# Performance work log

Hardware: AMD Instinct MI355X
Metric: run time of the kernel (lower is better)

The kernel has to match this reference:

```python
import jax, jax.numpy as jnp
import numpy as np

HEADS = 8
HEAD_DIM = 80
TEXT_LEN = 77


def setup_inputs() -> dict:
    key = jax.random.key(0)
    ks = jax.random.split(key, 10)
    B, S, QD, CD, ID = 16, 4096, 640, 768, 640
    NV = 10
    s = 0.02
    return {
        "x": jax.random.normal(ks[0], (B, S, QD), jnp.float32),
        "enc": jax.random.normal(ks[1], (B, TEXT_LEN + NV, CD), jnp.float32),
        "Wq": jax.random.normal(ks[2], (QD, ID), jnp.float32) * s,
        "Wvq": jax.random.normal(ks[3], (QD, ID), jnp.float32) * s,
        "Wk": jax.random.normal(ks[4], (CD, ID), jnp.float32) * s,
        "Wv": jax.random.normal(ks[5], (CD, ID), jnp.float32) * s,
        "Wvk": jax.random.normal(ks[6], (CD, ID), jnp.float32) * s,
        "Wvv": jax.random.normal(ks[7], (CD, ID), jnp.float32) * s,
        "Wo": jax.random.normal(ks[8], (ID, QD), jnp.float32) * s,
        "bo": jnp.zeros((QD,), jnp.float32),
    }


def reference(x, enc, Wq, Wvq, Wk, Wv, Wvk, Wvv, Wo, bo):
    # x: [B, S, query_dim]; enc: [B, 77 + Nv, cross_dim]
    B, S, _ = x.shape
    H, D = HEADS, HEAD_DIM
    scale = 1.0 / jnp.sqrt(jnp.asarray(D, x.dtype))

    text_feats = enc[:, :TEXT_LEN]      # [B, 77, CD]
    visual_feats = enc[:, TEXT_LEN:]    # [B, Nv, CD]

    tq = (x @ Wq).reshape(B, S, H, D)
    vq = (x @ Wvq).reshape(B, S, H, D)
    tk = (text_feats @ Wk).reshape(B, TEXT_LEN, H, D)
    tv = (text_feats @ Wv).reshape(B, TEXT_LEN, H, D)
    vk = (visual_feats @ Wvk).reshape(B, -1, H, D)
    vv = (visual_feats @ Wvv).reshape(B, -1, H, D)

    # separate score blocks, then concat along key dim
    text_scores = scale * jnp.einsum("bqhd,bkhd->bhqk", tq, tk)
    visual_scores = scale * jnp.einsum("bqhd,bkhd->bhqk", vq, vk)
    scores = jnp.concatenate([text_scores, visual_scores], axis=-1)  # [B,H,S,Kt+Kv]
    probs = jax.nn.softmax(scores, axis=-1)

    value = jnp.concatenate([tv, vv], axis=1)  # [B, Kt+Kv, H, D]
    out = jnp.einsum("bhqk,bkhd->bqhd", probs, value).reshape(B, S, H * D)
    return out @ Wo + bo
```

## Files before the change

kernel.cpp:

```cpp
#include <hip/hip_runtime.h>

typedef __attribute__((ext_vector_type(8))) short short8;
typedef __attribute__((ext_vector_type(4))) float f32x4;
typedef __attribute__((ext_vector_type(4))) int int4v;

typedef const __attribute__((address_space(1))) void* gas_t;
typedef __attribute__((address_space(3))) void* las_t;

__device__ __forceinline__ unsigned short f2bf(float f) {
  unsigned int u = __float_as_uint(f);
  u += 0x7fffu + ((u >> 16) & 1u);
  return (unsigned short)(u >> 16);
}

__global__ void cvt_bf16_kernel(const float* __restrict__ in,
                                unsigned short* __restrict__ out, int n) {
  int i = (blockIdx.x * 256 + threadIdx.x) * 4;
  if (i + 3 < n) {
    float4 v = *(const float4*)(in + i);
    ushort4 r;
    r.x = f2bf(v.x); r.y = f2bf(v.y); r.z = f2bf(v.z); r.w = f2bf(v.w);
    *(ushort4*)(out + i) = r;
  }
}

__global__ void transpose_cvt_kernel(const float* __restrict__ W,
                                     unsigned short* __restrict__ Wt,
                                     int K, int N) {
  __shared__ float t[32][33];
  int tx = threadIdx.x & 31, ty = threadIdx.x >> 5;
  int k0 = blockIdx.x * 32, n0 = blockIdx.y * 32;
  #pragma unroll
  for (int i = 0; i < 32; i += 8)
    t[ty + i][tx] = W[(size_t)(k0 + ty + i) * N + n0 + tx];
  __syncthreads();
  #pragma unroll
  for (int i = 0; i < 32; i += 8)
    Wt[(size_t)(n0 + ty + i) * K + k0 + tx] = f2bf(t[tx][ty + i]);
}

__global__ void vtrans_kernel(const unsigned short* __restrict__ KV,
                              unsigned short* __restrict__ VtG) {
  int idx = blockIdx.x * 256 + threadIdx.x;
  if (idx >= 16 * 8 * 80 * 96) return;
  int k = idx % 96;
  int d = (idx / 96) % 80;
  int h = (idx / (96 * 80)) % 8;
  int b = idx / (96 * 80 * 8);
  unsigned short v = 0;
  if (k < 87) {
    int base = (k < 77) ? 640 : 1920;
    v = KV[(size_t)(b * 87 + k) * 2560 + base + h * 80 + d];
  }
  VtG[idx] = v;
}

template<bool F32OUT>
__global__ __launch_bounds__(256, 2) void gemm_bt_kernel(
    const unsigned short* __restrict__ A,
    const unsigned short* __restrict__ Bt,
    void* __restrict__ Cptr, const float* __restrict__ bias,
    int M, int N, int K, int NT) {
  __shared__ __align__(16) unsigned short smem[2 * 128 * 64];
  unsigned short* As = smem;
  unsigned short* Bs = smem + 128 * 64;

  const int tid  = threadIdx.x;
  const int wave = tid >> 6, lane = tid & 63;
  const int lrow = lane & 15, quad = lane >> 4;

  const int nwg = gridDim.x;
  const int qch = nwg >> 3, rch = nwg & 7;
  const int xcd = blockIdx.x & 7;
  const int wgid = (xcd < rch ? xcd * (qch + 1)
                              : rch * (qch + 1) + (xcd - rch) * qch)
                 + (blockIdx.x >> 3);
  const int row0 = (wgid / NT) * 128, col0 = (wgid % NT) * 128;

  const int wm = (wave >> 1) * 64, wn = (wave & 1) * 64;
  const int srow = lane >> 3;
  const int scol = (lane & 7) * 8;

  f32x4 zero = {0.f, 0.f, 0.f, 0.f};
  f32x4 acc[4][4];
  #pragma unroll
  for (int mi = 0; mi < 4; ++mi)
    #pragma unroll
    for (int ni = 0; ni < 4; ++ni) acc[mi][ni] = zero;

  for (int k0 = 0; k0 < K; k0 += 64) {
    #pragma unroll
    for (int i = 0; i < 4; ++i) {
      int r = (wave * 4 + i) * 8 + srow;
      int ga = row0 + r; if (ga > M - 1) ga = M - 1;
      const unsigned short* gA = A + (size_t)ga * K + k0 + scol;
      __builtin_amdgcn_global_load_lds((gas_t)gA, (las_t)(As + r * 64 + scol), 16, 0, 0);
      const unsigned short* gB = Bt + (size_t)(col0 + r) * K + k0 + scol;
      __builtin_amdgcn_global_load_lds((gas_t)gB, (las_t)(Bs + r * 64 + scol), 16, 0, 0);
    }
    __syncthreads();
    #pragma unroll
    for (int kk = 0; kk < 64; kk += 32) {
      short8 av[4], bv[4];
      #pragma unroll
      for (int mi = 0; mi < 4; ++mi)
        av[mi] = *(const short8*)(As + (wm + mi * 16 + lrow) * 64 + kk + quad * 8);
      #pragma unroll
      for (int ni = 0; ni < 4; ++ni)
        bv[ni] = *(const short8*)(Bs + (wn + ni * 16 + lrow) * 64 + kk + quad * 8);
      #pragma unroll
      for (int mi = 0; mi < 4; ++mi)
        #pragma unroll
        for (int ni = 0; ni < 4; ++ni)
          acc[mi][ni] = __builtin_amdgcn_mfma_f32_16x16x32_bf16(av[mi], bv[ni], acc[mi][ni], 0, 0, 0);
    }
    __syncthreads();
  }

  if (F32OUT) {
    float* C = (float*)Cptr;
    #pragma unroll
    for (int mi = 0; mi < 4; ++mi)
      #pragma unroll
      for (int ni = 0; ni < 4; ++ni) {
        int col = col0 + wn + ni * 16 + lrow;
        float bv = bias[col];
        #pragma unroll
        for (int r = 0; r < 4; ++r) {
          int row = row0 + wm + mi * 16 + quad * 4 + r;
          if (row < M) C[(size_t)row * N + col] = acc[mi][ni][r] + bv;
        }
      }
  } else {
    unsigned short* C = (unsigned short*)Cptr;
    unsigned short* Cw = smem + wave * 4096;
    #pragma unroll
    for (int mi = 0; mi < 4; ++mi)
      #pragma unroll
      for (int ni = 0; ni < 4; ++ni)
        #pragma unroll
        for (int r = 0; r < 4; ++r)
          Cw[(mi * 16 + quad * 4 + r) * 64 + ni * 16 + lrow] = f2bf(acc[mi][ni][r]);
    #pragma unroll
    for (int it = 0; it < 8; ++it) {
      int row = it * 8 + (lane >> 3);
      int c8  = (lane & 7) * 8;
      int grow = row0 + wm + row;
      if (grow < M) {
        int4v v = *(const int4v*)(Cw + row * 64 + c8);
        *(int4v*)(C + (size_t)grow * N + col0 + wn + c8) = v;
      }
    }
  }
}

__global__ __launch_bounds__(256, 3) void attn_kernel(
    const unsigned short* __restrict__ Q,
    const unsigned short* __restrict__ KV,
    const unsigned short* __restrict__ VtG,
    unsigned short* __restrict__ O) {
  constexpr int KS = 168;
  constexpr int PS = 104;
  __shared__ __align__(16) unsigned short smem[96 * KS + 80 * PS];
  unsigned short* Ke = smem;
  unsigned short* Vt = smem + 96 * KS;
  unsigned short* P  = smem;

  const int tid = threadIdx.x;
  const int wave = tid >> 6, lane = tid & 63;
  const int lrow = lane & 15, quad = lane >> 4;
  const int qt = blockIdx.x, h = blockIdx.y, b = blockIdx.z;
  const size_t qbase = (size_t)(b * 4096 + qt * 64);

  const unsigned short* vg = VtG + (size_t)(b * 8 + h) * 80 * 96;
  for (int idx = tid; idx < 80 * 12; idx += 256) {
    int r = idx / 12, c = idx % 12;
    *(int4v*)(Vt + r * PS + c * 8) = *(const int4v*)(vg + r * 96 + c * 8);
  }
  for (int idx = tid; idx < 96 * 20; idx += 256) {
    int r = idx / 20, c = idx % 20;
    int4v v = {0, 0, 0, 0};
    if (r < 87) {
      if (r < 77 && c < 10)
        v = *(const int4v*)(KV + (size_t)(b * 87 + r) * 2560 + h * 80 + c * 8);
      else if (r >= 77 && c >= 10)
        v = *(const int4v*)(KV + (size_t)(b * 87 + r) * 2560 + 1280 + h * 80 + (c - 10) * 8);
    }
    *(int4v*)(Ke + r * KS + c * 8) = v;
  }

  const unsigned short* Qrow = Q + (qbase + wave * 16 + lrow) * 1280;
  short8 qfrag[5];
  #pragma unroll
  for (int kc = 0; kc < 5; ++kc) {
    int j = kc * 32 + quad * 8;
    int gcol = h * 80 + j + (j >= 80 ? 560 : 0);
    qfrag[kc] = *(const short8*)(Qrow + gcol);
  }
  __syncthreads();

  f32x4 zero = {0.f, 0.f, 0.f, 0.f};
  f32x4 s[6];
  #pragma unroll
  for (int nt = 0; nt < 6; ++nt) s[nt] = zero;
  #pragma unroll
  for (int kc = 0; kc < 5; ++kc) {
    #pragma unroll
    for (int nt = 0; nt < 6; ++nt) {
      short8 bb = *(const short8*)(Ke + (nt * 16 + lrow) * KS + kc * 32 + quad * 8);
      s[nt] = __builtin_amdgcn_mfma_f32_16x16x32_bf16(qfrag[kc], bb, s[nt], 0, 0, 0);
    }
  }

  const float scale = 0.11180339887498949f;
  float mrow[4] = {-1e30f, -1e30f, -1e30f, -1e30f};
  #pragma unroll
  for (int nt = 0; nt < 6; ++nt) {
    bool valid = (nt * 16 + lrow) < 87;
    #pragma unroll
    for (int r = 0; r < 4; ++r) {
      float v = valid ? s[nt][r] * scale : -1e30f;
      s[nt][r] = v;
      mrow[r] = fmaxf(mrow[r], v);
    }
  }
  #pragma unroll
  for (int off = 1; off < 16; off <<= 1)
    #pragma unroll
    for (int r = 0; r < 4; ++r)
      mrow[r] = fmaxf(mrow[r], __shfl_xor(mrow[r], off, 64));
  float lsum[4] = {0.f, 0.f, 0.f, 0.f};
  #pragma unroll
  for (int nt = 0; nt < 6; ++nt)
    #pragma unroll
    for (int r = 0; r < 4; ++r) {
      float p = __expf(s[nt][r] - mrow[r]);
      s[nt][r] = p;
      lsum[r] += p;
    }
  #pragma unroll
  for (int off = 1; off < 16; off <<= 1)
    #pragma unroll
    for (int r = 0; r < 4; ++r)
      lsum[r] += __shfl_xor(lsum[r], off, 64);
  float inv[4];
  #pragma unroll
  for (int r = 0; r < 4; ++r) inv[r] = 1.0f / lsum[r];

  __syncthreads();

  #pragma unroll
  for (int nt = 0; nt < 6; ++nt)
    #pragma unroll
    for (int r = 0; r < 4; ++r)
      P[(wave * 16 + quad * 4 + r) * PS + nt * 16 + lrow] = f2bf(s[nt][r] * inv[r]);

  f32x4 o[5];
  #pragma unroll
  for (int nt = 0; nt < 5; ++nt) o[nt] = zero;
  #pragma unroll
  for (int kc = 0; kc < 3; ++kc) {
    short8 a = *(const short8*)(P + (wave * 16 + lrow) * PS + kc * 32 + quad * 8);
    #pragma unroll
    for (int nt = 0; nt < 5; ++nt) {
      short8 bb = *(const short8*)(Vt + (nt * 16 + lrow) * PS + kc * 32 + quad * 8);
      o[nt] = __builtin_amdgcn_mfma_f32_16x16x32_bf16(a, bb, o[nt], 0, 0, 0);
    }
  }

  unsigned short* Ow = P + wave * 16 * PS;
  #pragma unroll
  for (int nt = 0; nt < 5; ++nt)
    #pragma unroll
    for (int r = 0; r < 4; ++r)
      Ow[(quad * 4 + r) * PS + nt * 16 + lrow] = f2bf(o[nt][r]);
  for (int idx = lane; idx < 160; idx += 64) {
    int r = idx / 10, c = idx % 10;
    *(int4v*)(O + (qbase + wave * 16 + r) * 640 + h * 80 + c * 8) =
        *(const int4v*)(Ow + r * PS + c * 8);
  }
}

extern "C" void kernel_launch(void* const* d_in, const int* in_sizes, int n_in,
                              void* d_out, int out_size, void* d_ws, size_t ws_size,
                              hipStream_t stream) {
  const float* x   = (const float*)d_in[0];
  const float* enc = (const float*)d_in[1];
  const float* Wq  = (const float*)d_in[2];
  const float* Wvq = (const float*)d_in[3];
  const float* Wk  = (const float*)d_in[4];
  const float* Wv  = (const float*)d_in[5];
  const float* Wvk = (const float*)d_in[6];
  const float* Wvv = (const float*)d_in[7];
  const float* Wo  = (const float*)d_in[8];
  const float* bo  = (const float*)d_in[9];
  float* out = (float*)d_out;
  char* ws = (char*)d_ws;

  unsigned short* Qall  = (unsigned short*)(ws);
  unsigned short* xbf   = (unsigned short*)(ws + 167772160ull);
  unsigned short* encbf = (unsigned short*)(ws + 251658240ull);
  unsigned short* KVall = (unsigned short*)(ws + 253796352ull);
  unsigned short* WqcT  = (unsigned short*)(ws + 260923392ull);
  unsigned short* WkvT  = (unsigned short*)(ws + 262561792ull);
  unsigned short* WoT   = (unsigned short*)(ws + 266493952ull);
  unsigned short* VtG   = WkvT;

  cvt_bf16_kernel<<<40960, 256, 0, stream>>>(x, xbf, 41943040);
  cvt_bf16_kernel<<<1044, 256, 0, stream>>>(enc, encbf, 1069056);

  transpose_cvt_kernel<<<dim3(20, 20), 256, 0, stream>>>(Wq,  WqcT,             640, 640);
  transpose_cvt_kernel<<<dim3(20, 20), 256, 0, stream>>>(Wvq, WqcT + 640 * 640, 640, 640);
  transpose_cvt_kernel<<<dim3(24, 20), 256, 0, stream>>>(Wk,  WkvT,              768, 640);
  transpose_cvt_kernel<<<dim3(24, 20), 256, 0, stream>>>(Wv,  WkvT + 640 * 768,  768, 640);
  transpose_cvt_kernel<<<dim3(24, 20), 256, 0, stream>>>(Wvk, WkvT + 1280 * 768, 768, 640);
  transpose_cvt_kernel<<<dim3(24, 20), 256, 0, stream>>>(Wvv, WkvT + 1920 * 768, 768, 640);
  transpose_cvt_kernel<<<dim3(20, 20), 256, 0, stream>>>(Wo,  WoT,              640, 640);

  gemm_bt_kernel<false><<<220, 256, 0, stream>>>(encbf, WkvT, KVall, nullptr, 1392, 2560, 768, 20);
  vtrans_kernel<<<3840, 256, 0, stream>>>(KVall, VtG);
  gemm_bt_kernel<false><<<5120, 256, 0, stream>>>(xbf, WqcT, Qall, nullptr, 65536, 1280, 640, 10);
  attn_kernel<<<dim3(64, 8, 16), 256, 0, stream>>>(Qall, KVall, VtG, xbf);
  gemm_bt_kernel<true><<<2560, 256, 0, stream>>>(xbf, WoT, out, bo, 65536, 640, 640, 5);
}
```

Measured before the change: 690.3 us.

## Add 256x256-tile 8-wave GEMM with 4-stage LDS pipeline for Q and output projections

Adds a new GEMM kernel that uses 256x256 output tiles, 512 threads, a 4-slot global_load_lds prefetch ring with three stages in flight, XCD-aware tile remapping and s_setprio around the MFMA blocks. The Q/visual-Q projection and the output projection now use this kernel instead of the 128-tile kernel. The aim is more operand reuse per byte loaded and better overlap of loads with compute on the large 65536-row GEMMs. In exchange it uses 128 KB of LDS and many accumulator registers per wave, which lowers occupancy. The output GEMM with N=640 leaves a partly empty last column tile, so some work is wasted.

```diff
diff --git a/kernel.cpp b/kernel.cpp
--- a/kernel.cpp
+++ b/kernel.cpp
@@ -143,6 +143,161 @@
           Cw[(mi * 16 + quad * 4 + r) * 64 + ni * 16 + lrow] = f2bf(acc[mi][ni][r]);
     #pragma unroll
     for (int it = 0; it < 8; ++it) {
+      int row = it * 8 + (lane >> 3);
+      int c8  = (lane & 7) * 8;
+      int grow = row0 + wm + row;
+      if (grow < M) {
+        int4v v = *(const int4v*)(Cw + row * 64 + c8);
+        *(int4v*)(C + (size_t)grow * N + col0 + wn + c8) = v;
+      }
+    }
+  }
+}
+
+template<bool F32OUT>
+__global__ __launch_bounds__(512, 2) void gemm256_kernel(
+    const unsigned short* __restrict__ A,
+    const unsigned short* __restrict__ Bt,
+    void* __restrict__ Cptr, const float* __restrict__ bias,
+    int M, int N, int K, int NT) {
+  __shared__ __align__(16) unsigned short smem[4 * 16384];
+
+  const int tid  = threadIdx.x;
+  const int wave = tid >> 6, lane = tid & 63;
+  const int lrow = lane & 15, quad = lane >> 4;
+
+  const int nwg = gridDim.x;
+  const int qch = nwg >> 3, rch = nwg & 7;
+  const int xcd = blockIdx.x & 7;
+  const int wgid = (xcd < rch ? xcd * (qch + 1)
+                              : rch * (qch + 1) + (xcd - rch) * qch)
+                 + (blockIdx.x >> 3);
+  const int row0 = (wgid / NT) * 256, col0 = (wgid % NT) * 256;
+
+  const int wm = (wave >> 2) * 128;
+  const int wn = (wave & 3) * 64;
+  const int NKT = K >> 5;
+
+  const unsigned short* gA[2];
+  const unsigned short* gB[2];
+  #pragma unroll
+  for (int j = 0; j < 2; ++j) {
+    int P = tid * 16 + j * 8192;
+    int lin = P ^ (((P >> 9) & 1) << 5);
+    int r = ((P >> 10) << 4) + ((lin >> 6) & 15);
+    int c = (lin & 63) >> 1;
+    int ga = row0 + r; if (ga > M - 1) ga = M - 1;
+    int gb = col0 + r; if (gb > N - 1) gb = N - 1;
+    gA[j] = A  + (size_t)ga * K + c;
+    gB[j] = Bt + (size_t)gb * K + c;
+  }
+
+  const int xorb = ((lrow >> 3) & 1) << 4;
+  int offA[8], offB[4];
+  #pragma unroll
+  for (int mi = 0; mi < 8; ++mi)
+    offA[mi] = (((((wm >> 4) + mi) << 9) + (lrow << 5) + (quad << 3))) ^ xorb;
+  #pragma unroll
+  for (int ni = 0; ni < 4; ++ni)
+    offB[ni] = (((((wn >> 4) + ni) << 9) + (lrow << 5) + (quad << 3))) ^ xorb;
+
+  f32x4 zero = {0.f, 0.f, 0.f, 0.f};
+  f32x4 acc[8][4];
+  #pragma unroll
+  for (int mi = 0; mi < 8; ++mi)
+    #pragma unroll
+    for (int ni = 0; ni < 4; ++ni) acc[mi][ni] = zero;
+
+  #pragma unroll
+  for (int t = 0; t < 3; ++t) {
+    unsigned short* slot = smem + (t & 3) * 16384;
+    #pragma unroll
+    for (int j = 0; j < 2; ++j)
+      __builtin_amdgcn_global_load_lds((gas_t)(gA[j] + t * 32),
+          (las_t)(slot + j * 4096 + tid * 8), 16, 0, 0);
+    #pragma unroll
+    for (int j = 0; j < 2; ++j)
+      __builtin_amdgcn_global_load_lds((gas_t)(gB[j] + t * 32),
+          (las_t)(slot + 8192 + j * 4096 + tid * 8), 16, 0, 0);
+  }
+
+  for (int t = 0; t < NKT; ++t) {
+    if (t + 2 < NKT)      asm volatile("s_waitcnt vmcnt(8)" ::: "memory");
+    else if (t + 1 < NKT) asm volatile("s_waitcnt vmcnt(4)" ::: "memory");
+    else                  asm volatile("s_waitcnt vmcnt(0)" ::: "memory");
+    asm volatile("s_barrier" ::: "memory");
+
+    const unsigned short* As = smem + (t & 3) * 16384;
+    const unsigned short* Bs = As + 8192;
+    const bool pf = (t + 3 < NKT);
+    unsigned short* nslot = smem + ((t + 3) & 3) * 16384;
+
+    short8 av0[4], bv[4];
+    #pragma unroll
+    for (int mi = 0; mi < 4; ++mi) av0[mi] = *(const short8*)(As + offA[mi]);
+    #pragma unroll
+    for (int ni = 0; ni < 4; ++ni) bv[ni] = *(const short8*)(Bs + offB[ni]);
+    if (pf) {
+      #pragma unroll
+      for (int j = 0; j < 2; ++j)
+        __builtin_amdgcn_global_load_lds((gas_t)(gA[j] + (t + 3) * 32),
+            (las_t)(nslot + j * 4096 + tid * 8), 16, 0, 0);
+    }
+    __builtin_amdgcn_s_setprio(1);
+    #pragma unroll
+    for (int mi = 0; mi < 4; ++mi)
+      #pragma unroll
+      for (int ni = 0; ni < 4; ++ni)
+        acc[mi][ni] = __builtin_amdgcn_mfma_f32_16x16x32_bf16(av0[mi], bv[ni], acc[mi][ni], 0, 0, 0);
+    __builtin_amdgcn_s_setprio(0);
+
+    short8 av1[4];
+    #pragma unroll
+    for (int mi = 0; mi < 4; ++mi) av1[mi] = *(const short8*)(As + offA[4 + mi]);
+    if (pf) {
+      #pragma unroll
+      for (int j = 0; j < 2; ++j)
+        __builtin_amdgcn_global_load_lds((gas_t)(gB[j] + (t + 3) * 32),
+            (las_t)(nslot + 8192 + j * 4096 + tid * 8), 16, 0, 0);
+    }
+    __builtin_amdgcn_s_setprio(1);
+    #pragma unroll
+    for (int mi = 0; mi < 4; ++mi)
+      #pragma unroll
+      for (int ni = 0; ni < 4; ++ni)
+        acc[4 + mi][ni] = __builtin_amdgcn_mfma_f32_16x16x32_bf16(av1[mi], bv[ni], acc[4 + mi][ni], 0, 0, 0);
+    __builtin_amdgcn_s_setprio(0);
+  }
+
+  if (F32OUT) {
+    float* C = (float*)Cptr;
+    #pragma unroll
+    for (int mi = 0; mi < 8; ++mi)
+      #pragma unroll
+      for (int ni = 0; ni < 4; ++ni) {
+        int col = col0 + wn + ni * 16 + lrow;
+        int colc = col < N ? col : 0;
+        float bval = bias[colc];
+        #pragma unroll
+        for (int r = 0; r < 4; ++r) {
+          int row = row0 + wm + mi * 16 + quad * 4 + r;
+          if (col < N && row < M)
+            C[(size_t)row * N + col] = acc[mi][ni][r] + bval;
+        }
+      }
+  } else {
+    asm volatile("s_barrier" ::: "memory");
+    unsigned short* C = (unsigned short*)Cptr;
+    unsigned short* Cw = smem + wave * 8192;
+    #pragma unroll
+    for (int mi = 0; mi < 8; ++mi)
+      #pragma unroll
+      for (int ni = 0; ni < 4; ++ni)
+        #pragma unroll
+        for (int r = 0; r < 4; ++r)
+          Cw[(mi * 16 + quad * 4 + r) * 64 + ni * 16 + lrow] = f2bf(acc[mi][ni][r]);
+    #pragma unroll
+    for (int it = 0; it < 16; ++it) {
       int row = it * 8 + (lane >> 3);
       int c8  = (lane & 7) * 8;
       int grow = row0 + wm + row;
@@ -319,7 +474,7 @@
 
   gemm_bt_kernel<false><<<220, 256, 0, stream>>>(encbf, WkvT, KVall, nullptr, 1392, 2560, 768, 20);
   vtrans_kernel<<<3840, 256, 0, stream>>>(KVall, VtG);
-  gemm_bt_kernel<false><<<5120, 256, 0, stream>>>(xbf, WqcT, Qall, nullptr, 65536, 1280, 640, 10);
+  gemm256_kernel<false><<<1280, 512, 0, stream>>>(xbf, WqcT, Qall, nullptr, 65536, 1280, 640, 5);
   attn_kernel<<<dim3(64, 8, 16), 256, 0, stream>>>(Qall, KVall, VtG, xbf);
-  gemm_bt_kernel<true><<<2560, 256, 0, stream>>>(xbf, WoT, out, bo, 65536, 640, 640, 5);
-}
+  gemm256_kernel<true><<<768, 512, 0, stream>>>(xbf, WoT, out, bo, 65536, 640, 640, 3);
+}
```

Result: faster. 650.0 us (-5.8%).
